# Optimization experiments

Hardware: AMD Instinct MI355X
Metric: run time of the kernel (lower is better)

The kernel has to match this reference:

```python
import jax, jax.numpy as jnp
import numpy as np

NTOKEN, NINP, DEPTH = 32000, 1024, 10
SEQ, BATCH = 128, 32


def setup_inputs() -> dict:
    key = jax.random.key(0)
    ks = jax.random.split(key, 10)
    initrange = 0.1
    inp = {
        "inputs": jax.random.randint(ks[0], (SEQ, BATCH), 0, NTOKEN),
        "h0": jnp.zeros((BATCH, NINP), jnp.float32),
        "c0": jnp.zeros((BATCH, NINP), jnp.float32),
        "memory0": jnp.zeros((BATCH, DEPTH, NINP), jnp.float32),
        # tied encoder/decoder weight, uniform(-0.1, 0.1) as in init_weights
        "enc_weight": jax.random.uniform(ks[1], (NTOKEN, NINP), jnp.float32, -initrange, initrange),
        "dec_bias": jnp.zeros((NTOKEN,), jnp.float32),
        # LSTMCell params (gate order i, f, g, o)
        "w_ih": jax.random.normal(ks[2], (4 * NINP, NINP), jnp.float32) * 0.02,
        "w_hh": jax.random.normal(ks[3], (4 * NINP, NINP), jnp.float32) * 0.02,
        "b_ih": jnp.zeros((4 * NINP,), jnp.float32),
        "b_hh": jnp.zeros((4 * NINP,), jnp.float32),
        # policy conv1d: (out=2, in=NINP, k=2)
        "conv_w": jax.random.normal(ks[4], (2, NINP, 2), jnp.float32) * 0.02,
        "conv_b": jnp.zeros((2,), jnp.float32),
        # policy linear: (2*(DEPTH+1), NINP)
        "pol_w": jax.random.normal(ks[5], (2 * (DEPTH + 1), NINP), jnp.float32) * 0.02,
        "pol_b": jnp.zeros((2 * (DEPTH + 1),), jnp.float32),
    }
    return inp


def _stack_rnn(inputs, h0, c0, memory0, enc_weight, dec_bias,
               w_ih, w_hh, b_ih, b_hh, conv_w, conv_b, pol_w, pol_b):
    B = h0.shape[0]
    N = h0.shape[1]
    D = memory0.shape[1]
    # shift index table: row k is memory shifted up by k positions
    shift_idx = jnp.arange(D + 1)[:, None] + jnp.arange(D)[None, :]  # [D+1, D]

    emb = enc_weight[inputs]  # [S, B, N]

    def step(carry, x):
        h, c, mem = carry
        # LSTM cell
        gates = x @ w_ih.T + b_ih + h @ w_hh.T + b_hh  # [B, 4N]
        i, f, g, o = jnp.split(gates, 4, axis=1)
        c = jax.nn.sigmoid(f) * c + jax.nn.sigmoid(i) * jnp.tanh(g)
        h = jax.nn.sigmoid(o) * jnp.tanh(c)
        # policy network: conv1d(k=2) over stack dim of memory padded by 2
        mem_p = jnp.pad(mem, ((0, 0), (0, 2), (0, 0)))  # [B, D+2, N]
        ps = (jnp.einsum('btn,on->bot', mem_p[:, :D + 1], conv_w[:, :, 0])
              + jnp.einsum('btn,on->bot', mem_p[:, 1:D + 2], conv_w[:, :, 1])
              + conv_b[None, :, None])  # [B, 2, D+1]
        logits = ps.reshape(B, 2 * (D + 1)) + x @ pol_w.T + pol_b
        policy = jax.nn.softmax(logits, axis=1)
        p_stay, p_push = policy[:, :D + 1], policy[:, D + 1:]
        # differentiable stack update (shift-register instead of eye-conv)
        mem_pad = jnp.pad(mem, ((0, 0), (0, D), (0, 0)))  # [B, 2D, N]
        m_stay = mem_pad[:, shift_idx]  # [B, D+1, D, N]
        pushed = jnp.broadcast_to(h[:, None, None, :], (B, D + 1, 1, N))
        m_push = jnp.concatenate([pushed, m_stay[:, :, :-1]], axis=2)  # [B, D+1, D, N]
        mem = (jnp.einsum('bk,bkdn->bdn', p_stay, m_stay)
               + jnp.einsum('bk,bkdn->bdn', p_push, m_push))
        return (h, c, mem), h

    (hT, cT, memT), hs = jax.lax.scan(step, (h0, c0, memory0), emb)
    decoded = hs @ enc_weight.T + dec_bias  # [S, B, NTOKEN]
    return decoded, (hT, cT), memT


def reference(inputs, h0, c0, memory0, enc_weight, dec_bias,
              w_ih, w_hh, b_ih, b_hh, conv_w, conv_b, pol_w, pol_b):
    return _stack_rnn(inputs, h0, c0, memory0, enc_weight, dec_bias,
                      w_ih, w_hh, b_ih, b_hh, conv_w, conv_b, pol_w, pol_b)
```

## Files before the change

### kernel.cpp

```cpp
#include <hip/hip_runtime.h>
#include <math.h>

#define SEQ    128
#define BATCH  32
#define NINP   1024
#define NGATE  4096
#define DEPTH  10
#define NPOL   22
#define NVOCAB 32000
#define DEC_OFF 131072000ll
#define NGB    64
#define NMB    32
#define NDB    160
#define XG_OFF 114294784

typedef __attribute__((ext_vector_type(8))) short bf16x8;
typedef __attribute__((ext_vector_type(4))) float f32x4;

__device__ __forceinline__ float sigf(float x){ return 1.0f/(1.0f + expf(-x)); }

__device__ __forceinline__ unsigned short f2bf(float x){
  unsigned int u = __float_as_uint(x);
  unsigned int r = (u + 0x7FFFu + ((u >> 16) & 1u)) >> 16;
  return (unsigned short)r;
}
__device__ __forceinline__ float bf2f(unsigned short u){
  return __uint_as_float(((unsigned int)u) << 16);
}

__global__ __launch_bounds__(256) void k_init(const float* __restrict__ h0,
    unsigned int* __restrict__ hsx0){
  int i = blockIdx.x*256 + threadIdx.x;
  unsigned int u = (unsigned int)f2bf(h0[2*i]) | ((unsigned int)f2bf(h0[2*i+1]) << 16);
  hsx0[i] = u;
}

__global__ __launch_bounds__(256) void k_wconv(const float* __restrict__ w_hh,
    unsigned short* __restrict__ w_swz){
  int id = blockIdx.x*256 + threadIdx.x;
  int lane = id & 63, kc = (id>>6)&7, kq = (id>>9)&3, nt = id>>11;
  int j = nt*16 + (lane&15);
  int k = kq*256 + kc*32 + (lane>>4)*8;
  const float* src = w_hh + (size_t)j*NINP + k;
  bf16x8 d;
  #pragma unroll
  for (int e=0;e<8;e++) d[e] = (short)f2bf(src[e]);
  *(bf16x8*)(w_swz + (size_t)id*8) = d;
}

__global__ __launch_bounds__(256) void k_enc(const float* __restrict__ enc,
    unsigned short* __restrict__ enc_bf){
  size_t gid = (size_t)blockIdx.x*256 + threadIdx.x;
  const float* s = enc + gid*16;
  float4 a0 = *(const float4*)(s);
  float4 a1 = *(const float4*)(s+4);
  float4 a2 = *(const float4*)(s+8);
  float4 a3 = *(const float4*)(s+12);
  bf16x8 o0, o1;
  o0[0]=f2bf(a0.x); o0[1]=f2bf(a0.y); o0[2]=f2bf(a0.z); o0[3]=f2bf(a0.w);
  o0[4]=f2bf(a1.x); o0[5]=f2bf(a1.y); o0[6]=f2bf(a1.z); o0[7]=f2bf(a1.w);
  o1[0]=f2bf(a2.x); o1[1]=f2bf(a2.y); o1[2]=f2bf(a2.z); o1[3]=f2bf(a2.w);
  o1[4]=f2bf(a3.x); o1[5]=f2bf(a3.y); o1[6]=f2bf(a3.z); o1[7]=f2bf(a3.w);
  *(bf16x8*)(enc_bf + gid*16)     = o0;
  *(bf16x8*)(enc_bf + gid*16 + 8) = o1;
}

__global__ __launch_bounds__(256) void k_gemm_bf16(
    const float* __restrict__ A, const int* __restrict__ Aidx,
    const float* __restrict__ B, const float* __restrict__ bias0,
    const float* __restrict__ bias1, float* __restrict__ C,
    int K, int ldc){
  __shared__ __align__(16) unsigned short As[128][40];
  __shared__ __align__(16) unsigned short Bs[128][40];
  const int m1 = blockIdx.y*128, n1 = blockIdx.x*128;
  const int tid = threadIdx.x;
  const int wave = tid >> 6, lane = tid & 63;
  const int wr = (wave >> 1) * 64, wc = (wave & 1) * 64;
  const int fr = lane & 15, fq = lane >> 4;

  f32x4 acc[4][4];
  #pragma unroll
  for (int i=0;i<4;i++)
    #pragma unroll
    for (int j=0;j<4;j++) acc[i][j] = (f32x4){0.f,0.f,0.f,0.f};

  const int sr = tid >> 1, sk = (tid & 1) * 16;
  const float* arow = Aidx ? (A + (size_t)Aidx[m1+sr]*K) : (A + (size_t)(m1+sr)*K);
  const float* brow = B + (size_t)(n1+sr)*K;

  for (int k0 = 0; k0 < K; k0 += 32){
    float4 a0 = *(const float4*)(arow + k0 + sk);
    float4 a1 = *(const float4*)(arow + k0 + sk + 4);
    float4 a2 = *(const float4*)(arow + k0 + sk + 8);
    float4 a3 = *(const float4*)(arow + k0 + sk + 12);
    float4 b0 = *(const float4*)(brow + k0 + sk);
    float4 b1 = *(const float4*)(brow + k0 + sk + 4);
    float4 b2 = *(const float4*)(brow + k0 + sk + 8);
    float4 b3 = *(const float4*)(brow + k0 + sk + 12);
    bf16x8 ap0, ap1, bp0, bp1;
    ap0[0]=f2bf(a0.x); ap0[1]=f2bf(a0.y); ap0[2]=f2bf(a0.z); ap0[3]=f2bf(a0.w);
    ap0[4]=f2bf(a1.x); ap0[5]=f2bf(a1.y); ap0[6]=f2bf(a1.z); ap0[7]=f2bf(a1.w);
    ap1[0]=f2bf(a2.x); ap1[1]=f2bf(a2.y); ap1[2]=f2bf(a2.z); ap1[3]=f2bf(a2.w);
    ap1[4]=f2bf(a3.x); ap1[5]=f2bf(a3.y); ap1[6]=f2bf(a3.z); ap1[7]=f2bf(a3.w);
    bp0[0]=f2bf(b0.x); bp0[1]=f2bf(b0.y); bp0[2]=f2bf(b0.z); bp0[3]=f2bf(b0.w);
    bp0[4]=f2bf(b1.x); bp0[5]=f2bf(b1.y); bp0[6]=f2bf(b1.z); bp0[7]=f2bf(b1.w);
    bp1[0]=f2bf(b2.x); bp1[1]=f2bf(b2.y); bp1[2]=f2bf(b2.z); bp1[3]=f2bf(b2.w);
    bp1[4]=f2bf(b3.x); bp1[5]=f2bf(b3.y); bp1[6]=f2bf(b3.z); bp1[7]=f2bf(b3.w);

    __syncthreads();
    *(bf16x8*)&As[sr][sk]     = ap0;
    *(bf16x8*)&As[sr][sk + 8] = ap1;
    *(bf16x8*)&Bs[sr][sk]     = bp0;
    *(bf16x8*)&Bs[sr][sk + 8] = bp1;
    __syncthreads();

    bf16x8 af[4], bf[4];
    #pragma unroll
    for (int mi=0; mi<4; mi++) af[mi] = *(const bf16x8*)&As[wr + mi*16 + fr][fq*8];
    #pragma unroll
    for (int ni=0; ni<4; ni++) bf[ni] = *(const bf16x8*)&Bs[wc + ni*16 + fr][fq*8];
    #pragma unroll
    for (int mi=0; mi<4; mi++)
      #pragma unroll
      for (int ni=0; ni<4; ni++)
        acc[mi][ni] = __builtin_amdgcn_mfma_f32_16x16x32_bf16(af[mi], bf[ni], acc[mi][ni], 0, 0, 0);
  }

  #pragma unroll
  for (int ni=0; ni<4; ni++){
    const int col = n1 + wc + ni*16 + fr;
    const float bv = (bias0 ? bias0[col] : 0.f) + (bias1 ? bias1[col] : 0.f);
    #pragma unroll
    for (int mi=0; mi<4; mi++){
      const int row0 = m1 + wr + mi*16 + fq*4;
      #pragma unroll
      for (int j=0; j<4; j++)
        C[(size_t)(row0 + j)*ldc + col] = acc[mi][ni][j] + bv;
    }
  }
}

__global__ __launch_bounds__(256) void k_gemm_dec(
    const unsigned short* __restrict__ A, const float* __restrict__ B,
    const float* __restrict__ bias, float* __restrict__ C){
  __shared__ __align__(16) unsigned short As[128][40];
  __shared__ __align__(16) unsigned short Bs[128][40];
  const int m1 = blockIdx.x*128, n1 = blockIdx.y*128;
  const int tid = threadIdx.x;
  const int wave = tid >> 6, lane = tid & 63;
  const int wr = (wave >> 1) * 64, wc = (wave & 1) * 64;
  const int fr = lane & 15, fq = lane >> 4;

  f32x4 acc[4][4];
  #pragma unroll
  for (int i=0;i<4;i++)
    #pragma unroll
    for (int j=0;j<4;j++) acc[i][j] = (f32x4){0.f,0.f,0.f,0.f};

  const int sr = tid >> 1, sk = (tid & 1) * 16;
  const unsigned short* arow = A + (size_t)(m1+sr)*NINP;
  const float* brow = B + (size_t)(n1+sr)*NINP;

  for (int k0 = 0; k0 < NINP; k0 += 32){
    bf16x8 ap0 = *(const bf16x8*)(arow + k0 + sk);
    bf16x8 ap1 = *(const bf16x8*)(arow + k0 + sk + 8);
    float4 b0 = *(const float4*)(brow + k0 + sk);
    float4 b1 = *(const float4*)(brow + k0 + sk + 4);
    float4 b2 = *(const float4*)(brow + k0 + sk + 8);
    float4 b3 = *(const float4*)(brow + k0 + sk + 12);
    bf16x8 bp0, bp1;
    bp0[0]=f2bf(b0.x); bp0[1]=f2bf(b0.y); bp0[2]=f2bf(b0.z); bp0[3]=f2bf(b0.w);
    bp0[4]=f2bf(b1.x); bp0[5]=f2bf(b1.y); bp0[6]=f2bf(b1.z); bp0[7]=f2bf(b1.w);
    bp1[0]=f2bf(b2.x); bp1[1]=f2bf(b2.y); bp1[2]=f2bf(b2.z); bp1[3]=f2bf(b2.w);
    bp1[4]=f2bf(b3.x); bp1[5]=f2bf(b3.y); bp1[6]=f2bf(b3.z); bp1[7]=f2bf(b3.w);

    __syncthreads();
    *(bf16x8*)&As[sr][sk]     = ap0;
    *(bf16x8*)&As[sr][sk + 8] = ap1;
    *(bf16x8*)&Bs[sr][sk]     = bp0;
    *(bf16x8*)&Bs[sr][sk + 8] = bp1;
    __syncthreads();

    bf16x8 af[4], bf[4];
    #pragma unroll
    for (int mi=0; mi<4; mi++) af[mi] = *(const bf16x8*)&As[wr + mi*16 + fr][fq*8];
    #pragma unroll
    for (int ni=0; ni<4; ni++) bf[ni] = *(const bf16x8*)&Bs[wc + ni*16 + fr][fq*8];
    #pragma unroll
    for (int mi=0; mi<4; mi++)
      #pragma unroll
      for (int ni=0; ni<4; ni++)
        acc[mi][ni] = __builtin_amdgcn_mfma_f32_16x16x32_bf16(af[mi], bf[ni], acc[mi][ni], 0, 0, 0);
  }

  #pragma unroll
  for (int ni=0; ni<4; ni++){
    const int col = n1 + wc + ni*16 + fr;
    const float bv = bias[col];
    #pragma unroll
    for (int mi=0; mi<4; mi++){
      const int row0 = m1 + wr + mi*16 + fq*4;
      #pragma unroll
      for (int j=0; j<4; j++)
        C[(size_t)(row0 + j)*NVOCAB + col] = acc[mi][ni][j] + bv;
    }
  }
}

__global__ __launch_bounds__(256) void k_xp(const float* __restrict__ enc,
    const int* __restrict__ inputs, const float* __restrict__ pol_w,
    const float* __restrict__ pol_b, const float* __restrict__ conv_b,
    float* __restrict__ logit_base){
  const int m = blockIdx.x;
  const float* x = enc + (size_t)inputs[m]*NINP;
  __shared__ float xs[NINP];
  for (int i=threadIdx.x; i<NINP; i+=256) xs[i] = x[i];
  __syncthreads();
  const int wave = threadIdx.x >> 6, lane = threadIdx.x & 63;
  for (int p = wave; p < NPOL; p += 4){
    const float* w = pol_w + (size_t)p*NINP;
    float s = 0.f;
    for (int k=lane; k<NINP; k+=64) s = fmaf(xs[k], w[k], s);
    #pragma unroll
    for (int off=32; off; off>>=1) s += __shfl_down(s, off);
    if (lane==0) logit_base[(size_t)m*NPOL + p] = s + pol_b[p] + conv_b[p/11];
  }
}

#define ARRIVE(VAL)                                                                     \
  __syncthreads();                                                                      \
  if (tid == 0){                                                                        \
    __builtin_amdgcn_fence(__ATOMIC_RELEASE, "agent");                                  \
    __hip_atomic_store(flags + blk*16, (VAL), __ATOMIC_RELAXED, __HIP_MEMORY_SCOPE_AGENT); \
  }
#define WAITH_S(VAL, SLP)                                                               \
  if (tid < 64){                                                                        \
    int v_ = __hip_atomic_load(flags + tid*16, __ATOMIC_RELAXED, __HIP_MEMORY_SCOPE_AGENT); \
    while (__ballot(v_ < (VAL)) != 0ull){                                               \
      __builtin_amdgcn_s_sleep(SLP);                                                    \
      v_ = __hip_atomic_load(flags + tid*16, __ATOMIC_RELAXED, __HIP_MEMORY_SCOPE_AGENT); \
    }                                                                                   \
    if (tid == 0) __builtin_amdgcn_fence(__ATOMIC_ACQUIRE, "agent");                    \
  }                                                                                     \
  __syncthreads();
#define WAITH(VAL) WAITH_S(VAL, 1)

__global__ __launch_bounds__(256, 1) void k_scan(
    const float* __restrict__ xg, const unsigned short* __restrict__ w_swz,
    const float* __restrict__ conv_w, const float* __restrict__ lbase,
    unsigned int* __restrict__ hsx, const float* __restrict__ c0,
    const float* __restrict__ m0, float* __restrict__ ot, int* __restrict__ flags,
    const unsigned short* __restrict__ enc_bf, const float* __restrict__ dbias,
    float* __restrict__ Cout){
  const int blk = blockIdx.x, tid = threadIdx.x;

  __shared__ __align__(16) unsigned short hlds[32*1024];
  __shared__ float gl[32][68];

  if (blk < NGB){
    const int wv = tid >> 6, lane = tid & 63;
    const int fr = lane & 15, fq = lane >> 4;
    const int n0 = blk * 16;
    bf16x8 wreg[32];
    {
      const unsigned short* wb = w_swz + ((size_t)(wv*64 + blk)*32*64 + (size_t)lane)*8;
      #pragma unroll
      for (int ks=0; ks<32; ks++) wreg[ks] = *(const bf16x8*)(wb + (size_t)ks*512);
    }
    const int eb = tid >> 3, ej0 = (tid & 7)*2, en0 = n0 + ej0;
    float creg0 = c0[eb*NINP + en0], creg1 = c0[eb*NINP + en0 + 1];

    for (int t=0; t<SEQ; ++t){
      const float* xr = xg + ((size_t)t*BATCH + eb)*NGATE + en0;
      const float2 x_i = *(const float2*)(xr);
      const float2 x_f = *(const float2*)(xr + NINP);
      const float2 x_g = *(const float2*)(xr + 2*NINP);
      const float2 x_o = *(const float2*)(xr + 3*NINP);

      WAITH(t)

      {
        const unsigned short* hsrc = (const unsigned short*)(hsx + (size_t)t*16384);
        const int sb = tid >> 3, seg = tid & 7;
        const bf16x8* src = (const bf16x8*)(hsrc + sb*NINP);
        #pragma unroll
        for (int i=0;i<16;i++){
          int ch = seg*16 + i;
          ((bf16x8*)hlds)[sb*128 + (ch ^ (sb&7))] = src[ch];
        }
      }
      __syncthreads();

      f32x4 acc0 = {0.f,0.f,0.f,0.f}, acc1 = {0.f,0.f,0.f,0.f};
      #pragma unroll
      for (int ks=0; ks<32; ks++){
        bf16x8 a0 = ((const bf16x8*)hlds)[fr*128      + ((ks*4 + fq) ^ (fr&7))];
        bf16x8 a1 = ((const bf16x8*)hlds)[(16+fr)*128 + ((ks*4 + fq) ^ (fr&7))];
        acc0 = __builtin_amdgcn_mfma_f32_16x16x32_bf16(a0, wreg[ks], acc0, 0,0,0);
        acc1 = __builtin_amdgcn_mfma_f32_16x16x32_bf16(a1, wreg[ks], acc1, 0,0,0);
      }
      #pragma unroll
      for (int r=0;r<4;r++){
        gl[fq*4 + r][wv*16 + fr]      = acc0[r];
        gl[16 + fq*4 + r][wv*16 + fr] = acc1[r];
      }
      __syncthreads();

      {
        float gi0 = sigf (gl[eb][ej0]      + x_i.x), gi1 = sigf (gl[eb][ej0+1]      + x_i.y);
        float gf0 = sigf (gl[eb][16+ej0]   + x_f.x), gf1 = sigf (gl[eb][16+ej0+1]   + x_f.y);
        float gg0 = tanhf(gl[eb][32+ej0]   + x_g.x), gg1 = tanhf(gl[eb][32+ej0+1]   + x_g.y);
        float go0 = sigf (gl[eb][48+ej0]   + x_o.x), go1 = sigf (gl[eb][48+ej0+1]   + x_o.y);
        float cc0 = gf0*creg0 + gi0*gg0,  cc1 = gf1*creg1 + gi1*gg1;
        float hh0 = go0*tanhf(cc0),       hh1 = go1*tanhf(cc1);
        creg0 = cc0; creg1 = cc1;
        unsigned int pk = (unsigned int)f2bf(hh0) | ((unsigned int)f2bf(hh1) << 16);
        hsx[(size_t)(t+1)*16384 + eb*512 + (en0>>1)] = pk;
        if (t == SEQ-1){
          ot[eb*NINP + en0] = hh0;  ot[eb*NINP + en0 + 1] = hh1;
          ot[BATCH*NINP + eb*NINP + en0] = cc0;
          ot[BATCH*NINP + eb*NINP + en0 + 1] = cc1;
        }
      }
      ARRIVE(t+1)
    }
  } else if (blk < NGB + NMB) {
    const int b = blk - NGB;
    const int wv = tid >> 6, lane = tid & 63;
    const int col0 = tid*4;
    __shared__ float red[NPOL][4];
    __shared__ float sp[NPOL];
    float m[4][DEPTH];
    #pragma unroll
    for (int c=0;c<4;c++)
      #pragma unroll
      for (int d=0;d<DEPTH;d++) m[c][d] = m0[(size_t)b*DEPTH*NINP + d*NINP + col0 + c];
    float cw0[2][4], cw1[2][4];
    #pragma unroll
    for (int o=0;o<2;o++)
      #pragma unroll
      for (int c=0;c<4;c++){
        cw0[o][c] = conv_w[o*2*NINP + 2*(col0+c)];
        cw1[o][c] = conv_w[o*2*NINP + 2*(col0+c) + 1];
      }

    for (int t=0; t<SEQ; ++t){
      float lp[NPOL];
      #pragma unroll
      for (int o=0;o<2;o++)
        #pragma unroll
        for (int tp=0; tp<11; tp++){
          float v = 0.f;
          #pragma unroll
          for (int c=0;c<4;c++){
            if (tp < DEPTH)   v = fmaf(m[c][tp],   cw0[o][c], v);
            if (tp+1 < DEPTH) v = fmaf(m[c][tp+1], cw1[o][c], v);
          }
          lp[o*11+tp] = v;
        }
      #pragma unroll
      for (int p=0;p<NPOL;p++){
        #pragma unroll
        for (int off=32; off; off>>=1) lp[p] += __shfl_down(lp[p], off);
      }
      if (lane == 0){
        #pragma unroll
        for (int p=0;p<NPOL;p++) red[p][wv] = lp[p];
      }
      __syncthreads();
      if (tid == 0){
        float l[NPOL]; float mx = -1e30f;
        #pragma unroll
        for (int p=0;p<NPOL;p++){
          l[p] = red[p][0]+red[p][1]+red[p][2]+red[p][3]
               + lbase[(size_t)t*(BATCH*NPOL) + b*NPOL + p];
          mx = fmaxf(mx, l[p]);
        }
        float sum = 0.f;
        #pragma unroll
        for (int p=0;p<NPOL;p++){ l[p] = expf(l[p]-mx); sum += l[p]; }
        float inv = 1.f/sum;
        #pragma unroll
        for (int p=0;p<NPOL;p++) sp[p] = l[p]*inv;
      }
      WAITH(t+1)

      const unsigned short* hsrc = (const unsigned short*)(hsx + (size_t)(t+1)*16384);
      unsigned long long hv = *(const unsigned long long*)(hsrc + b*NINP + col0);
      float hc[4];
      hc[0] = bf2f((unsigned short)hv);
      hc[1] = bf2f((unsigned short)(hv >> 16));
      hc[2] = bf2f((unsigned short)(hv >> 32));
      hc[3] = bf2f((unsigned short)(hv >> 48));

      float psum = 0.f;
      #pragma unroll
      for (int k2=11;k2<22;k2++) psum += sp[k2];
      #pragma unroll
      for (int c=0;c<4;c++){
        float outv[DEPTH];
        {
          float v = psum*hc[c];
          #pragma unroll
          for (int jj=0;jj<DEPTH;jj++) v = fmaf(sp[jj], m[c][jj], v);
          outv[0] = v;
        }
        #pragma unroll
        for (int d=1; d<DEPTH; d++){
          float v = 0.f;
          for (int jj=d;   jj<DEPTH; jj++) v = fmaf(sp[jj-d],    m[c][jj], v);
          for (int jj=d-1; jj<DEPTH; jj++) v = fmaf(sp[12+jj-d], m[c][jj], v);
          outv[d] = v;
        }
        #pragma unroll
        for (int d=0;d<DEPTH;d++) m[c][d] = outv[d];
      }
      __syncthreads();
      if (t == SEQ-1){
        #pragma unroll
        for (int c=0;c<4;c++)
          #pragma unroll
          for (int d=0;d<DEPTH;d++)
            ot[2*BATCH*NINP + (size_t)b*DEPTH*NINP + d*NINP + col0 + c] = m[c][d];
      }
    }
  } else {
    const int wave = tid >> 6, lane = tid & 63;
    const int wr = (wave >> 1) * 64, wc = (wave & 1) * 64;
    const int fr = lane & 15, fq = lane >> 4;
    unsigned short* As = (unsigned short*)hlds;
    unsigned short* Bs = As + 128*128;
    const unsigned short* hsA = (const unsigned short*)(hsx + 16384);
    const int srow0 = wave*32;
    const int lrow = lane >> 4;
    const int lch  = lane & 15;
    int fenced = 0;
    const int dBlk = blk - (NGB + NMB);

    for (int tile = dBlk; tile < 32*250; tile += NDB){
      const int mt = tile/250, nt = tile - mt*250;
      const int req = 4*mt + 4;
      if (req > fenced){ WAITH_S(req, 8); fenced = req; }
      const int m1 = mt*128, n1 = nt*128;

      f32x4 acc[4][4];
      #pragma unroll
      for (int i=0;i<4;i++)
        #pragma unroll
        for (int j=0;j<4;j++) acc[i][j] = (f32x4){0.f,0.f,0.f,0.f};

      for (int k0 = 0; k0 < NINP; k0 += 128){
        __syncthreads();
        #pragma unroll
        for (int j=0;j<8;j++){
          const int r = srow0 + j*4 + lrow;
          const unsigned short* gA = hsA + (size_t)(m1 + r)*NINP + k0 + (lch ^ (r&7))*8;
          __builtin_amdgcn_global_load_lds((const unsigned int*)gA,
              (unsigned int*)(As + (size_t)(srow0 + j*4)*128), 16, 0, 0);
        }
        #pragma unroll
        for (int j=0;j<8;j++){
          const int r = srow0 + j*4 + lrow;
          const unsigned short* gB = enc_bf + (size_t)(n1 + r)*NINP + k0 + (lch ^ (r&7))*8;
          __builtin_amdgcn_global_load_lds((const unsigned int*)gB,
              (unsigned int*)(Bs + (size_t)(srow0 + j*4)*128), 16, 0, 0);
        }
        __syncthreads();

        #pragma unroll
        for (int ks=0; ks<4; ks++){
          bf16x8 af[4], bf[4];
          #pragma unroll
          for (int mi=0; mi<4; mi++){
            const int r = wr + mi*16 + fr;
            af[mi] = *(const bf16x8*)(As + (size_t)r*128 + ((ks*4 + fq) ^ (r&7))*8);
          }
          #pragma unroll
          for (int ni=0; ni<4; ni++){
            const int r = wc + ni*16 + fr;
            bf[ni] = *(const bf16x8*)(Bs + (size_t)r*128 + ((ks*4 + fq) ^ (r&7))*8);
          }
          #pragma unroll
          for (int mi=0; mi<4; mi++)
            #pragma unroll
            for (int ni=0; ni<4; ni++)
              acc[mi][ni] = __builtin_amdgcn_mfma_f32_16x16x32_bf16(af[mi], bf[ni], acc[mi][ni], 0, 0, 0);
        }
      }

      #pragma unroll
      for (int ni=0; ni<4; ni++){
        const int col = n1 + wc + ni*16 + fr;
        const float bv = dbias[col];
        #pragma unroll
        for (int mi=0; mi<4; mi++){
          const int row0 = m1 + wr + mi*16 + fq*4;
          #pragma unroll
          for (int j=0; j<4; j++)
            Cout[(size_t)(row0 + j)*NVOCAB + col] = acc[mi][ni][j] + bv;
        }
      }
    }
  }
}

extern "C" void kernel_launch(void* const* d_in, const int* in_sizes, int n_in,
                              void* d_out, int out_size, void* d_ws, size_t ws_size,
                              hipStream_t stream){
  (void)in_sizes; (void)n_in; (void)out_size;
  const int*   inputs = (const int*)  d_in[0];
  const float* h0     = (const float*)d_in[1];
  const float* c0     = (const float*)d_in[2];
  const float* m0     = (const float*)d_in[3];
  const float* enc    = (const float*)d_in[4];
  const float* dbias  = (const float*)d_in[5];
  const float* w_ih   = (const float*)d_in[6];
  const float* w_hh   = (const float*)d_in[7];
  const float* b_ih   = (const float*)d_in[8];
  const float* b_hh   = (const float*)d_in[9];
  const float* conv_w = (const float*)d_in[10];
  const float* conv_b = (const float*)d_in[11];
  const float* pol_w  = (const float*)d_in[12];
  const float* pol_b  = (const float*)d_in[13];

  float* out = (float*)d_out;
  float* ws  = (float*)d_ws;
  float* lbase = ws;
  unsigned int* hsx = (unsigned int*)(ws + 90112);
  unsigned short* hs_bf  = (unsigned short*)(hsx + 16384);
  unsigned short* enc_bf = (unsigned short*)(ws + 90112 + 2113536);
  int* flags_ws          = (int*)(ws + 90112 + 2113536 + 16384000);
  const int overlap = (ws_size >= (size_t)18600000*4);
  float* xg = overlap ? (out + XG_OFF) : out;
  unsigned short* w_swz = (unsigned short*)(out + 17000000);
  int* flags = overlap ? flags_ws : (int*)(out + 19600000);
  float* ot = out + DEC_OFF;

  k_init<<<64, 256, 0, stream>>>(h0, hsx);
  k_wconv<<<2048, 256, 0, stream>>>(w_hh, w_swz);
  if (overlap) k_enc<<<8000, 256, 0, stream>>>(enc, enc_bf);

  dim3 gxg(32, 32);
  k_gemm_bf16<<<gxg, 256, 0, stream>>>(enc, inputs, w_ih, b_ih, b_hh, xg, NINP, NGATE);

  k_xp<<<SEQ*BATCH, 256, 0, stream>>>(enc, inputs, pol_w, pol_b, conv_b, lbase);

  hipMemsetAsync(flags, 0, 64*16*sizeof(int), stream);

  const int nblk = overlap ? (NGB + NMB + NDB) : (NGB + NMB);
  k_scan<<<nblk, 256, 0, stream>>>(xg, w_swz, conv_w, lbase, hsx, c0, m0,
                                   ot, flags, enc_bf, dbias, out);

  if (!overlap){
    dim3 gdec(32, 250);
    k_gemm_dec<<<gdec, 256, 0, stream>>>(hs_bf, enc, dbias, out);
  }
}
```

Before: 1.385 ms.

## Fold embedding bf16 conversion into decoder blocks and map roles by XCD

Drops the separate k_enc kernel that converted the 32000x1024 embedding to bf16. The decoder-role blocks inside the persistent scan kernel now do that conversion themselves, then meet at a global atomic counter before starting their GEMM tiles, so the conversion runs alongside the LSTM recurrence instead of ahead of it. Block roles are also reassigned by blockIdx modulo 8, so gate blocks sit on two XCDs, memory blocks on one and decoder blocks on the other five. The cost is a grid-wide spin barrier among the decoder blocks, and the conversion traffic now competes for bandwidth with the latency-critical recurrence.

```diff
diff --git a/kernel.cpp b/kernel.cpp
--- a/kernel.cpp
+++ b/kernel.cpp
@@ -46,23 +46,6 @@
   #pragma unroll
   for (int e=0;e<8;e++) d[e] = (short)f2bf(src[e]);
   *(bf16x8*)(w_swz + (size_t)id*8) = d;
-}
-
-__global__ __launch_bounds__(256) void k_enc(const float* __restrict__ enc,
-    unsigned short* __restrict__ enc_bf){
-  size_t gid = (size_t)blockIdx.x*256 + threadIdx.x;
-  const float* s = enc + gid*16;
-  float4 a0 = *(const float4*)(s);
-  float4 a1 = *(const float4*)(s+4);
-  float4 a2 = *(const float4*)(s+8);
-  float4 a3 = *(const float4*)(s+12);
-  bf16x8 o0, o1;
-  o0[0]=f2bf(a0.x); o0[1]=f2bf(a0.y); o0[2]=f2bf(a0.z); o0[3]=f2bf(a0.w);
-  o0[4]=f2bf(a1.x); o0[5]=f2bf(a1.y); o0[6]=f2bf(a1.z); o0[7]=f2bf(a1.w);
-  o1[0]=f2bf(a2.x); o1[1]=f2bf(a2.y); o1[2]=f2bf(a2.z); o1[3]=f2bf(a2.w);
-  o1[4]=f2bf(a3.x); o1[5]=f2bf(a3.y); o1[6]=f2bf(a3.z); o1[7]=f2bf(a3.w);
-  *(bf16x8*)(enc_bf + gid*16)     = o0;
-  *(bf16x8*)(enc_bf + gid*16 + 8) = o1;
 }
 
 __global__ __launch_bounds__(256) void k_gemm_bf16(
@@ -227,11 +210,11 @@
   }
 }
 
-#define ARRIVE(VAL)                                                                     \
+#define ARRIVE(ID, VAL)                                                                 \
   __syncthreads();                                                                      \
   if (tid == 0){                                                                        \
     __builtin_amdgcn_fence(__ATOMIC_RELEASE, "agent");                                  \
-    __hip_atomic_store(flags + blk*16, (VAL), __ATOMIC_RELAXED, __HIP_MEMORY_SCOPE_AGENT); \
+    __hip_atomic_store(flags + (ID)*16, (VAL), __ATOMIC_RELAXED, __HIP_MEMORY_SCOPE_AGENT); \
   }
 #define WAITH_S(VAL, SLP)                                                               \
   if (tid < 64){                                                                        \
@@ -251,19 +234,31 @@
     unsigned int* __restrict__ hsx, const float* __restrict__ c0,
     const float* __restrict__ m0, float* __restrict__ ot, int* __restrict__ flags,
     const unsigned short* __restrict__ enc_bf, const float* __restrict__ dbias,
-    float* __restrict__ Cout){
+    float* __restrict__ Cout, const float* __restrict__ enc, int part){
   const int blk = blockIdx.x, tid = threadIdx.x;
+
+  int role, rid;
+  if (part){
+    const int xcd = blk & 7, slot = blk >> 3;
+    if (xcd < 2)      { role = 0; rid = slot*2 + xcd; }
+    else if (xcd == 2){ role = 1; rid = slot; }
+    else              { role = 2; rid = slot*5 + (xcd-3); }
+  } else {
+    role = (blk < NGB) ? 0 : 1;
+    rid  = (blk < NGB) ? blk : (blk - NGB);
+  }
 
   __shared__ __align__(16) unsigned short hlds[32*1024];
   __shared__ float gl[32][68];
 
-  if (blk < NGB){
+  if (role == 0){
+    const int gid = rid;
     const int wv = tid >> 6, lane = tid & 63;
     const int fr = lane & 15, fq = lane >> 4;
-    const int n0 = blk * 16;
+    const int n0 = gid * 16;
     bf16x8 wreg[32];
     {
-      const unsigned short* wb = w_swz + ((size_t)(wv*64 + blk)*32*64 + (size_t)lane)*8;
+      const unsigned short* wb = w_swz + ((size_t)(wv*64 + gid)*32*64 + (size_t)lane)*8;
       #pragma unroll
       for (int ks=0; ks<32; ks++) wreg[ks] = *(const bf16x8*)(wb + (size_t)ks*512);
     }
@@ -322,10 +317,10 @@
           ot[BATCH*NINP + eb*NINP + en0 + 1] = cc1;
         }
       }
-      ARRIVE(t+1)
-    }
-  } else if (blk < NGB + NMB) {
-    const int b = blk - NGB;
+      ARRIVE(gid, t+1)
+    }
+  } else if (role == 1) {
+    const int b = rid;
     const int wv = tid >> 6, lane = tid & 63;
     const int col0 = tid*4;
     __shared__ float red[NPOL][4];
@@ -425,6 +420,36 @@
       }
     }
   } else {
+    const int dBlk = rid;
+    int* ecnt = flags + 1024;
+
+    {
+      unsigned short* ebw = (unsigned short*)enc_bf;
+      for (int it = dBlk*256 + tid; it < 2048000; it += NDB*256){
+        const float* s = enc + (size_t)it*16;
+        float4 a0 = *(const float4*)(s);
+        float4 a1 = *(const float4*)(s+4);
+        float4 a2 = *(const float4*)(s+8);
+        float4 a3 = *(const float4*)(s+12);
+        bf16x8 o0, o1;
+        o0[0]=f2bf(a0.x); o0[1]=f2bf(a0.y); o0[2]=f2bf(a0.z); o0[3]=f2bf(a0.w);
+        o0[4]=f2bf(a1.x); o0[5]=f2bf(a1.y); o0[6]=f2bf(a1.z); o0[7]=f2bf(a1.w);
+        o1[0]=f2bf(a2.x); o1[1]=f2bf(a2.y); o1[2]=f2bf(a2.z); o1[3]=f2bf(a2.w);
+        o1[4]=f2bf(a3.x); o1[5]=f2bf(a3.y); o1[6]=f2bf(a3.z); o1[7]=f2bf(a3.w);
+        *(bf16x8*)(ebw + (size_t)it*16)     = o0;
+        *(bf16x8*)(ebw + (size_t)it*16 + 8) = o1;
+      }
+      __syncthreads();
+      if (tid == 0){
+        __builtin_amdgcn_fence(__ATOMIC_RELEASE, "agent");
+        __hip_atomic_fetch_add(ecnt, 1, __ATOMIC_RELAXED, __HIP_MEMORY_SCOPE_AGENT);
+        while (__hip_atomic_load(ecnt, __ATOMIC_RELAXED, __HIP_MEMORY_SCOPE_AGENT) < NDB)
+          __builtin_amdgcn_s_sleep(8);
+        __builtin_amdgcn_fence(__ATOMIC_ACQUIRE, "agent");
+      }
+      __syncthreads();
+    }
+
     const int wave = tid >> 6, lane = tid & 63;
     const int wr = (wave >> 1) * 64, wc = (wave & 1) * 64;
     const int fr = lane & 15, fq = lane >> 4;
@@ -435,7 +460,6 @@
     const int lrow = lane >> 4;
     const int lch  = lane & 15;
     int fenced = 0;
-    const int dBlk = blk - (NGB + NMB);
 
     for (int tile = dBlk; tile < 32*250; tile += NDB){
       const int mt = tile/250, nt = tile - mt*250;
@@ -538,18 +562,17 @@
 
   k_init<<<64, 256, 0, stream>>>(h0, hsx);
   k_wconv<<<2048, 256, 0, stream>>>(w_hh, w_swz);
-  if (overlap) k_enc<<<8000, 256, 0, stream>>>(enc, enc_bf);
 
   dim3 gxg(32, 32);
   k_gemm_bf16<<<gxg, 256, 0, stream>>>(enc, inputs, w_ih, b_ih, b_hh, xg, NINP, NGATE);
 
   k_xp<<<SEQ*BATCH, 256, 0, stream>>>(enc, inputs, pol_w, pol_b, conv_b, lbase);
 
-  hipMemsetAsync(flags, 0, 64*16*sizeof(int), stream);
+  hipMemsetAsync(flags, 0, (64*16 + 16)*sizeof(int), stream);
 
   const int nblk = overlap ? (NGB + NMB + NDB) : (NGB + NMB);
   k_scan<<<nblk, 256, 0, stream>>>(xg, w_swz, conv_w, lbase, hsx, c0, m0,
-                                   ot, flags, enc_bf, dbias, out);
+                                   ot, flags, enc_bf, dbias, out, enc, overlap);
 
   if (!overlap){
     dim3 gdec(32, 250);
```

New measurement: 2.259 ms. +63.1%, slower.
